# Kernel optimization log

Hardware: AMD Instinct MI355X
Metric: run time of the kernel (lower is better)

The kernel has to match this reference:

```python
import jax, jax.numpy as jnp
import numpy as np

DIM = 1024
HEADS = 16
HEAD_DIM = DIM // HEADS
B, N = 4, 4096


def setup_inputs() -> dict:
    key = jax.random.key(0)
    k1, k2, k3, k4, k5 = jax.random.split(key, 5)
    scale_in = 1.0 / np.sqrt(DIM)
    return {
        "x": jax.random.normal(k1, (B, N, DIM), dtype=jnp.float32),
        # torch nn.Linear convention: weight [out, in], y = x @ W.T + b
        "w_qkv": jax.random.uniform(k2, (3 * DIM, DIM), jnp.float32, -scale_in, scale_in),
        "b_qkv": jax.random.uniform(k3, (3 * DIM,), jnp.float32, -scale_in, scale_in),
        "w_proj": jax.random.uniform(k4, (DIM, DIM), jnp.float32, -scale_in, scale_in),
        "b_proj": jax.random.uniform(k5, (DIM,), jnp.float32, -scale_in, scale_in),
    }


def reference(x, w_qkv, b_qkv, w_proj, b_proj):
    Bx, Nx, C = x.shape
    H, D = HEADS, HEAD_DIM
    qkv = (x @ w_qkv.T + b_qkv).reshape(Bx, Nx, 3, H, D)
    q, k, v = qkv[:, :, 0], qkv[:, :, 1], qkv[:, :, 2]  # each [B, N, H, D]
    # NOTE: faithful to source — heads dim was NOT moved to batch position,
    # so attention mixes across heads per token: scores [B, N, H, H].
    scores = jnp.einsum('bnhd,bngd->bnhg', q, k) / jnp.sqrt(jnp.asarray(D, x.dtype))
    attn = jax.nn.softmax(scores, axis=-1)
    out = jnp.einsum('bnhg,bngd->bnhd', attn, v).reshape(Bx, Nx, C)
    return out @ w_proj.T + b_proj
```

## Files before the change

### kernel.cpp

```cpp
#include <hip/hip_runtime.h>
#include <hip/hip_bf16.h>
#include <stdint.h>

typedef __bf16 v8bf __attribute__((ext_vector_type(8)));
typedef float  v4f  __attribute__((ext_vector_type(4)));
typedef unsigned short u16;

#define NTOK 16384
#define KDIM 1024

__device__ __forceinline__ u16 f2bf(float f) {
  uint32_t b = __builtin_bit_cast(uint32_t, f);
  b += 0x7FFFu + ((b >> 16) & 1u);
  return (u16)(b >> 16);
}

__device__ __forceinline__ void gl_lds16(const u16* g, u16* l) {
  __builtin_amdgcn_global_load_lds(
      (const __attribute__((address_space(1))) uint32_t*)g,
      (__attribute__((address_space(3))) uint32_t*)l,
      16, 0, 0);
}

__device__ __forceinline__ void bar() {
  __builtin_amdgcn_sched_barrier(0);
  __builtin_amdgcn_s_barrier();
  __builtin_amdgcn_sched_barrier(0);
}
#define LGKM0() do { asm volatile("s_waitcnt lgkmcnt(0)" ::: "memory"); \
                     __builtin_amdgcn_sched_barrier(0); } while (0)
#define VMW(n)  do { asm volatile("s_waitcnt vmcnt(" #n ")" ::: "memory"); \
                     __builtin_amdgcn_sched_barrier(0); } while (0)

__global__ void cvt_bf16(const float* __restrict__ in, u16* __restrict__ out) {
  size_t i = ((size_t)blockIdx.x * 256 + threadIdx.x) * 8;
  float4 a = *(const float4*)(in + i);
  float4 b = *(const float4*)(in + i + 4);
  union { u16 u[8]; uint4 v; } pk;
  pk.u[0]=f2bf(a.x); pk.u[1]=f2bf(a.y); pk.u[2]=f2bf(a.z); pk.u[3]=f2bf(a.w);
  pk.u[4]=f2bf(b.x); pk.u[5]=f2bf(b.y); pk.u[6]=f2bf(b.z); pk.u[7]=f2bf(b.w);
  *(uint4*)(out + i) = pk.v;
}

template<int NTOT, bool OUT_BF16>
__global__ __launch_bounds__(512, 2)
void gemm_bt(const u16* __restrict__ A, const u16* __restrict__ Bw,
             const float* __restrict__ bias, void* __restrict__ out) {
  constexpr int NM = NTOK / 256;
  constexpr int NN = NTOT / 256;
  constexpr int NWG = NM * NN;
  constexpr int NT = KDIM / 32;
  const int bid = blockIdx.x;
  const int swz = (bid & 7) * (NWG / 8) + (bid >> 3);
  const int bm = swz % NM, bn = swz / NM;

  __shared__ __align__(16) u16 lds[2][2][256 * 32];

  const int tid = threadIdx.x, lane = tid & 63, w = tid >> 6;
  const int wr = w >> 2, wc = w & 3;

  v4f acc[8][4];
#pragma unroll
  for (int i = 0; i < 8; ++i)
#pragma unroll
    for (int j = 0; j < 4; ++j) acc[i][j] = v4f{0.f, 0.f, 0.f, 0.f};

  const u16* Ab = A  + (size_t)bm * 256 * KDIM;
  const u16* Bb = Bw + (size_t)bn * 256 * KDIM;

  const size_t soff = (size_t)(tid >> 2) * KDIM
      + (size_t)((((tid & 3) ^ ((tid >> 2) & 3) ^ ((tid >> 4) & 3)) & 3) * 8);
  auto stage = [&](u16* dst, const u16* src) { gl_lds16(src + soff, dst + tid * 8); };

  const int cks = ((lane >> 4) ^ (lane & 3) ^ ((lane >> 2) & 3)) & 3;
  const int aoff = (wr * 128 + (lane & 15)) * 32 + cks * 8;
  const int boff = (wc * 64  + (lane & 15)) * 32 + cks * 8;

#define QUAD(MF0, NF0) do {                                              \
  _Pragma("unroll") for (int qi = 0; qi < 4; ++qi)                       \
  _Pragma("unroll") for (int qj = 0; qj < 2; ++qj)                       \
    acc[(MF0)+qi][(NF0)+qj] = __builtin_amdgcn_mfma_f32_16x16x32_bf16(   \
        af[(MF0)+qi], bfr[(NF0)+qj], acc[(MF0)+qi][(NF0)+qj], 0, 0, 0);  \
} while (0)

  stage(&lds[0][0][0], Ab);
  stage(&lds[0][0][4096], Ab + 128 * KDIM);
  stage(&lds[0][1][0], Bb);
  stage(&lds[0][1][4096], Bb + 128 * KDIM);
  stage(&lds[1][0][0], Ab + 32);
  stage(&lds[1][0][4096], Ab + 128 * KDIM + 32);
  VMW(2);
  bar();

  for (int t = 0; t < NT; ++t) {
    const int p = t & 1;
    const u16* La = lds[p][0];
    const u16* Lb = lds[p][1];
    u16* Sb = lds[p ^ 1][1];
    u16* Sa = lds[p][0];
    const u16* Bs = Bb + (size_t)(t + 1) * 32;
    const u16* As = Ab + (size_t)(t + 2) * 32;
    v8bf af[8], bfr[4];

#pragma unroll
    for (int f = 0; f < 4; ++f) af[f] = *(const v8bf*)(La + aoff + f * 512);
#pragma unroll
    for (int f = 0; f < 2; ++f) bfr[f] = *(const v8bf*)(Lb + boff + f * 512);
    if (t + 1 < NT) stage(Sb, Bs);
    bar(); LGKM0();
    __builtin_amdgcn_s_setprio(1); QUAD(0, 0); __builtin_amdgcn_s_setprio(0);
    bar();

#pragma unroll
    for (int f = 4; f < 8; ++f) af[f] = *(const v8bf*)(La + aoff + f * 512);
#pragma unroll
    for (int f = 2; f < 4; ++f) bfr[f] = *(const v8bf*)(Lb + boff + f * 512);
    if (t + 1 < NT) stage(Sb + 4096, Bs + 128 * KDIM);
    bar(); LGKM0();
    __builtin_amdgcn_s_setprio(1); QUAD(4, 2); __builtin_amdgcn_s_setprio(0);
    bar();

    if (t + 2 < NT) stage(Sa, As);
    bar();
    __builtin_amdgcn_s_setprio(1); QUAD(0, 2); __builtin_amdgcn_s_setprio(0);
    bar();

    if (t + 2 < NT) stage(Sa + 4096, As + 128 * KDIM);
    bar();
    __builtin_amdgcn_s_setprio(1); QUAD(4, 0); __builtin_amdgcn_s_setprio(0);
    if (t + 2 < NT) { VMW(2); } else { VMW(0); }
    bar();
  }
#undef QUAD

  const int col0 = bn * 256 + wc * 64 + (lane & 15);
  const int row0 = bm * 256 + wr * 128 + ((lane >> 4) << 2);
#pragma unroll
  for (int mf = 0; mf < 8; ++mf) {
#pragma unroll
    for (int nf = 0; nf < 4; ++nf) {
      const int gc = col0 + nf * 16;
      const float bv = bias[gc];
#pragma unroll
      for (int j = 0; j < 4; ++j) {
        const size_t idx = (size_t)(row0 + mf * 16 + j) * NTOT + gc;
        const float v = acc[mf][nf][j] + bv;
        if constexpr (OUT_BF16) ((u16*)out)[idx] = f2bf(v);
        else                    ((float*)out)[idx] = v;
      }
    }
  }
}

__global__ __launch_bounds__(256)
void attn_mix(const u16* __restrict__ qkv, u16* __restrict__ outp) {
  __shared__ __align__(16) u16 sq[4][3072];
  __shared__ float sp[4][16][16];
  const int tid = threadIdx.x, lane = tid & 63, w = tid >> 6;
  const size_t tok = (size_t)blockIdx.x * 4 + w;
  const u16* src = qkv + tok * 3072;
#pragma unroll
  for (int i = 0; i < 6; ++i) {
    int t = i * 64 + lane;
    int row = t >> 3;
    int c = (t & 7) ^ (row & 7);
    gl_lds16(src + row * 64 + c * 8, &sq[w][t * 8]);
  }
  __syncthreads();

  const int h = lane >> 2, gb = lane & 3;
  v8bf qv[8];
#pragma unroll
  for (int c = 0; c < 8; ++c)
    qv[c] = *(const v8bf*)&sq[w][h * 64 + ((c ^ (h & 7)) * 8)];

  float s[4];
#pragma unroll
  for (int g4 = 0; g4 < 4; ++g4) {
    const int g = gb * 4 + g4;
    float a = 0.f;
#pragma unroll
    for (int c = 0; c < 8; ++c) {
      v8bf kv = *(const v8bf*)&sq[w][1024 + g * 64 + ((c ^ (g & 7)) * 8)];
#pragma unroll
      for (int j = 0; j < 8; ++j) a += (float)qv[c][j] * (float)kv[j];
    }
    s[g4] = a * 0.125f;
  }
  float m = fmaxf(fmaxf(s[0], s[1]), fmaxf(s[2], s[3]));
  m = fmaxf(m, __shfl_xor(m, 1));
  m = fmaxf(m, __shfl_xor(m, 2));
  float p[4], sum = 0.f;
#pragma unroll
  for (int g4 = 0; g4 < 4; ++g4) { p[g4] = __expf(s[g4] - m); sum += p[g4]; }
  sum += __shfl_xor(sum, 1);
  sum += __shfl_xor(sum, 2);
  const float inv = 1.f / sum;
#pragma unroll
  for (int g4 = 0; g4 < 4; ++g4) sp[w][h][gb * 4 + g4] = p[g4] * inv;
  __syncthreads();

  float o[16];
#pragma unroll
  for (int j = 0; j < 16; ++j) o[j] = 0.f;
  const int db = gb;
#pragma unroll
  for (int g = 0; g < 16; ++g) {
    const float a = sp[w][h][g];
    v8bf v0 = *(const v8bf*)&sq[w][2048 + g * 64 + (((db * 2)     ^ (g & 7)) * 8)];
    v8bf v1 = *(const v8bf*)&sq[w][2048 + g * 64 + (((db * 2 + 1) ^ (g & 7)) * 8)];
#pragma unroll
    for (int j = 0; j < 8; ++j) { o[j] += a * (float)v0[j]; o[8 + j] += a * (float)v1[j]; }
  }
  union { u16 u[16]; uint4 v[2]; } ob;
#pragma unroll
  for (int j = 0; j < 16; ++j) ob.u[j] = f2bf(o[j]);
  u16* dst = outp + tok * 1024 + h * 64 + db * 16;
  *(uint4*)dst = ob.v[0];
  *((uint4*)dst + 1) = ob.v[1];
}

extern "C" void kernel_launch(void* const* d_in, const int* in_sizes, int n_in,
                              void* d_out, int out_size, void* d_ws, size_t ws_size,
                              hipStream_t stream) {
  const float* x      = (const float*)d_in[0];
  const float* w_qkv  = (const float*)d_in[1];
  const float* b_qkv  = (const float*)d_in[2];
  const float* w_proj = (const float*)d_in[3];
  const float* b_proj = (const float*)d_in[4];

  char* ws = (char*)d_ws;
  u16* x_bf    = (u16*)(ws);
  u16* wqkv_bf = (u16*)(ws + (size_t)33554432);
  u16* wp_bf   = (u16*)(ws + (size_t)39845888);
  u16* qkv_bf  = (u16*)(ws + (size_t)41943040);
  u16* at_bf   = (u16*)(ws + (size_t)142606336);

  cvt_bf16<<<dim3(8192), dim3(256), 0, stream>>>(x, x_bf);
  cvt_bf16<<<dim3(1536), dim3(256), 0, stream>>>(w_qkv, wqkv_bf);
  cvt_bf16<<<dim3(512),  dim3(256), 0, stream>>>(w_proj, wp_bf);

  gemm_bt<3072, true ><<<dim3(768), dim3(512), 0, stream>>>(x_bf, wqkv_bf, b_qkv, qkv_bf);
  attn_mix<<<dim3(4096), dim3(256), 0, stream>>>(qkv_bf, at_bf);
  gemm_bt<1024, false><<<dim3(256), dim3(512), 0, stream>>>(at_bf, wp_bf, b_proj, d_out);
}
```

Baseline: 239.9 us.

## Restructure GEMM K-loop into two half-steps and fuse bf16 conversion launches

The GEMM main loop is rewritten as two half-steps per K tile. All four B fragments are loaded once, and each half runs a 4x4 MFMA block. The next A tile and a later B tile are prefetched at new points, which cuts the barriers and LDS fragment reloads per K step. The three fp32-to-bf16 conversion kernels are merged into a single launch that branches on the global thread index. The new buffer-reuse ordering depends on barrier placement being right, and holding more fragments raises register pressure.

```diff
diff --git a/kernel.cpp b/kernel.cpp
--- a/kernel.cpp
+++ b/kernel.cpp
@@ -32,14 +32,20 @@
 #define VMW(n)  do { asm volatile("s_waitcnt vmcnt(" #n ")" ::: "memory"); \
                      __builtin_amdgcn_sched_barrier(0); } while (0)
 
-__global__ void cvt_bf16(const float* __restrict__ in, u16* __restrict__ out) {
-  size_t i = ((size_t)blockIdx.x * 256 + threadIdx.x) * 8;
-  float4 a = *(const float4*)(in + i);
-  float4 b = *(const float4*)(in + i + 4);
+__global__ void cvt_all(const float* __restrict__ x, const float* __restrict__ wq,
+                        const float* __restrict__ wp, u16* __restrict__ xo,
+                        u16* __restrict__ wqo, u16* __restrict__ wpo) {
+  size_t id = (size_t)blockIdx.x * 256 + threadIdx.x;
+  const float* src; u16* dst;
+  if (id < 2097152)      { src = x  + id * 8;              dst = xo  + id * 8; }
+  else if (id < 2490368) { src = wq + (id - 2097152) * 8;  dst = wqo + (id - 2097152) * 8; }
+  else                   { src = wp + (id - 2490368) * 8;  dst = wpo + (id - 2490368) * 8; }
+  float4 a = *(const float4*)(src);
+  float4 b = *(const float4*)(src + 4);
   union { u16 u[8]; uint4 v; } pk;
   pk.u[0]=f2bf(a.x); pk.u[1]=f2bf(a.y); pk.u[2]=f2bf(a.z); pk.u[3]=f2bf(a.w);
   pk.u[4]=f2bf(b.x); pk.u[5]=f2bf(b.y); pk.u[6]=f2bf(b.z); pk.u[7]=f2bf(b.w);
-  *(uint4*)(out + i) = pk.v;
+  *(uint4*)(dst) = pk.v;
 }
 
 template<int NTOT, bool OUT_BF16>
@@ -68,70 +74,59 @@
   const u16* Ab = A  + (size_t)bm * 256 * KDIM;
   const u16* Bb = Bw + (size_t)bn * 256 * KDIM;
 
-  const size_t soff = (size_t)(tid >> 2) * KDIM
+  const size_t soff0 = (size_t)(tid >> 2) * KDIM
       + (size_t)((((tid & 3) ^ ((tid >> 2) & 3) ^ ((tid >> 4) & 3)) & 3) * 8);
-  auto stage = [&](u16* dst, const u16* src) { gl_lds16(src + soff, dst + tid * 8); };
+  auto stage2 = [&](u16* dst, const u16* src) {
+    gl_lds16(src + soff0, dst + (size_t)tid * 8);
+    gl_lds16(src + soff0 + (size_t)128 * KDIM, dst + (size_t)tid * 8 + 4096);
+  };
 
   const int cks = ((lane >> 4) ^ (lane & 3) ^ ((lane >> 2) & 3)) & 3;
   const int aoff = (wr * 128 + (lane & 15)) * 32 + cks * 8;
   const int boff = (wc * 64  + (lane & 15)) * 32 + cks * 8;
 
-#define QUAD(MF0, NF0) do {                                              \
-  _Pragma("unroll") for (int qi = 0; qi < 4; ++qi)                       \
-  _Pragma("unroll") for (int qj = 0; qj < 2; ++qj)                       \
-    acc[(MF0)+qi][(NF0)+qj] = __builtin_amdgcn_mfma_f32_16x16x32_bf16(   \
-        af[(MF0)+qi], bfr[(NF0)+qj], acc[(MF0)+qi][(NF0)+qj], 0, 0, 0);  \
+#define HALFSTEP(CUR, TA, TB) do {                                            \
+  const u16* La_ = lds[CUR][0];                                               \
+  const u16* Lb_ = lds[CUR][1];                                               \
+  v8bf af[4], bf4[4];                                                         \
+  _Pragma("unroll") for (int f = 0; f < 4; ++f)                               \
+    af[f] = *(const v8bf*)(La_ + aoff + f * 512);                             \
+  _Pragma("unroll") for (int f = 0; f < 4; ++f)                               \
+    bf4[f] = *(const v8bf*)(Lb_ + boff + f * 512);                            \
+  if ((TA) < NT) stage2(&lds[(CUR) ^ 1][0][0], Ab + (size_t)(TA) * 32);       \
+  bar(); LGKM0();                                                             \
+  __builtin_amdgcn_s_setprio(1);                                              \
+  _Pragma("unroll") for (int qi = 0; qi < 4; ++qi)                            \
+  _Pragma("unroll") for (int qj = 0; qj < 4; ++qj)                            \
+    acc[qi][qj] = __builtin_amdgcn_mfma_f32_16x16x32_bf16(                    \
+        af[qi], bf4[qj], acc[qi][qj], 0, 0, 0);                               \
+  __builtin_amdgcn_s_setprio(0);                                              \
+  bar();                                                                      \
+  _Pragma("unroll") for (int f = 0; f < 4; ++f)                               \
+    af[f] = *(const v8bf*)(La_ + aoff + (f + 4) * 512);                       \
+  if ((TB) < NT) stage2(&lds[CUR][1][0], Bb + (size_t)(TB) * 32);             \
+  bar(); LGKM0();                                                             \
+  __builtin_amdgcn_s_setprio(1);                                              \
+  _Pragma("unroll") for (int qi = 0; qi < 4; ++qi)                            \
+  _Pragma("unroll") for (int qj = 0; qj < 4; ++qj)                            \
+    acc[4 + qi][qj] = __builtin_amdgcn_mfma_f32_16x16x32_bf16(                \
+        af[qi], bf4[qj], acc[4 + qi][qj], 0, 0, 0);                           \
+  __builtin_amdgcn_s_setprio(0);                                              \
+  if ((TB) < NT) { VMW(2); } else { VMW(0); }                                 \
+  bar();                                                                      \
 } while (0)
 
-  stage(&lds[0][0][0], Ab);
-  stage(&lds[0][0][4096], Ab + 128 * KDIM);
-  stage(&lds[0][1][0], Bb);
-  stage(&lds[0][1][4096], Bb + 128 * KDIM);
-  stage(&lds[1][0][0], Ab + 32);
-  stage(&lds[1][0][4096], Ab + 128 * KDIM + 32);
+  stage2(&lds[0][1][0], Bb);
+  stage2(&lds[0][0][0], Ab);
+  stage2(&lds[1][1][0], Bb + 32);
   VMW(2);
   bar();
 
-  for (int t = 0; t < NT; ++t) {
-    const int p = t & 1;
-    const u16* La = lds[p][0];
-    const u16* Lb = lds[p][1];
-    u16* Sb = lds[p ^ 1][1];
-    u16* Sa = lds[p][0];
-    const u16* Bs = Bb + (size_t)(t + 1) * 32;
-    const u16* As = Ab + (size_t)(t + 2) * 32;
-    v8bf af[8], bfr[4];
-
-#pragma unroll
-    for (int f = 0; f < 4; ++f) af[f] = *(const v8bf*)(La + aoff + f * 512);
-#pragma unroll
-    for (int f = 0; f < 2; ++f) bfr[f] = *(const v8bf*)(Lb + boff + f * 512);
-    if (t + 1 < NT) stage(Sb, Bs);
-    bar(); LGKM0();
-    __builtin_amdgcn_s_setprio(1); QUAD(0, 0); __builtin_amdgcn_s_setprio(0);
-    bar();
-
-#pragma unroll
-    for (int f = 4; f < 8; ++f) af[f] = *(const v8bf*)(La + aoff + f * 512);
-#pragma unroll
-    for (int f = 2; f < 4; ++f) bfr[f] = *(const v8bf*)(Lb + boff + f * 512);
-    if (t + 1 < NT) stage(Sb + 4096, Bs + 128 * KDIM);
-    bar(); LGKM0();
-    __builtin_amdgcn_s_setprio(1); QUAD(4, 2); __builtin_amdgcn_s_setprio(0);
-    bar();
-
-    if (t + 2 < NT) stage(Sa, As);
-    bar();
-    __builtin_amdgcn_s_setprio(1); QUAD(0, 2); __builtin_amdgcn_s_setprio(0);
-    bar();
-
-    if (t + 2 < NT) stage(Sa + 4096, As + 128 * KDIM);
-    bar();
-    __builtin_amdgcn_s_setprio(1); QUAD(4, 0); __builtin_amdgcn_s_setprio(0);
-    if (t + 2 < NT) { VMW(2); } else { VMW(0); }
-    bar();
-  }
-#undef QUAD
+  for (int j = 0; j < NT / 2; ++j) {
+    HALFSTEP(0, 2 * j + 1, 2 * j + 2);
+    HALFSTEP(1, 2 * j + 2, 2 * j + 3);
+  }
+#undef HALFSTEP
 
   const int col0 = bn * 256 + wc * 64 + (lane & 15);
   const int row0 = bm * 256 + wr * 128 + ((lane >> 4) << 2);
@@ -236,9 +231,8 @@
   u16* qkv_bf  = (u16*)(ws + (size_t)41943040);
   u16* at_bf   = (u16*)(ws + (size_t)142606336);
 
-  cvt_bf16<<<dim3(8192), dim3(256), 0, stream>>>(x, x_bf);
-  cvt_bf16<<<dim3(1536), dim3(256), 0, stream>>>(w_qkv, wqkv_bf);
-  cvt_bf16<<<dim3(512),  dim3(256), 0, stream>>>(w_proj, wp_bf);
+  cvt_all<<<dim3(10240), dim3(256), 0, stream>>>(x, w_qkv, w_proj,
+                                                 x_bf, wqkv_bf, wp_bf);
 
   gemm_bt<3072, true ><<<dim3(768), dim3(512), 0, stream>>>(x_bf, wqkv_bf, b_qkv, qkv_bf);
   attn_mix<<<dim3(4096), dim3(256), 0, stream>>>(qkv_bf, at_bf);
```

Result: faster. 221.9 us (-7.5%).
